# Optimization experiments

Measured on AMD Instinct MI355X. Metric: run time of the kernel, lower is better.

Reference implementation:

```python
import jax, jax.numpy as jnp
import numpy as np

D, W, H = 128, 128, 128          # volume obj_shape (d, w, h)
RES_SCALE = 1.4
RES_D = int(D * RES_SCALE)       # 179 detector rows
RES_H = int(H * RES_SCALE)       # 179 detector cols
N_PROJ = 10


def setup_inputs() -> dict:
    key = jax.random.key(0)
    k1, k2 = jax.random.split(key, 2)
    # learnable reconstruction volume, initialized to ones (torch.ones_like)
    I_rec = jnp.ones((1, 1, D, W, H), dtype=jnp.float32)
    # emitter positions, scaled to volume size; y-component kept away from the
    # source plane y=0 so that ray directions are well-conditioned
    poses = jax.random.uniform(k1, (50, 3), dtype=jnp.float32)
    poses = poses * jnp.array([D, W, H], jnp.float32) + jnp.array([-64.0, 256.0, -64.0], jnp.float32)
    idx = jax.random.randint(k2, (N_PROJ,), 0, 50, dtype=jnp.int32)
    return {"I_rec": I_rec, "poses": poses, "idx": idx}


def _trilinear_3d(vol, coords):
    """torch F.grid_sample 3D, bilinear, align_corners=False, zero padding.
    vol: [D, Hd, Wd]; coords: [..., 3] in (x, y, z) normalized to [-1, 1],
    where x indexes the last (Wd) axis, y the middle, z the first."""
    Dv, Hv, Wv = vol.shape
    x, y, z = coords[..., 0], coords[..., 1], coords[..., 2]
    ix = ((x + 1.0) * Wv - 1.0) * 0.5
    iy = ((y + 1.0) * Hv - 1.0) * 0.5
    iz = ((z + 1.0) * Dv - 1.0) * 0.5
    x0f, y0f, z0f = jnp.floor(ix), jnp.floor(iy), jnp.floor(iz)
    tx, ty, tz = ix - x0f, iy - y0f, iz - z0f
    x0 = x0f.astype(jnp.int32); y0 = y0f.astype(jnp.int32); z0 = z0f.astype(jnp.int32)
    x1, y1, z1 = x0 + 1, y0 + 1, z0 + 1

    def gather(zc, yc, xc):
        valid = (zc >= 0) & (zc < Dv) & (yc >= 0) & (yc < Hv) & (xc >= 0) & (xc < Wv)
        v = vol[jnp.clip(zc, 0, Dv - 1), jnp.clip(yc, 0, Hv - 1), jnp.clip(xc, 0, Wv - 1)]
        return jnp.where(valid, v, 0.0)

    out = (
        gather(z0, y0, x0) * (1 - tz) * (1 - ty) * (1 - tx)
        + gather(z0, y0, x1) * (1 - tz) * (1 - ty) * tx
        + gather(z0, y1, x0) * (1 - tz) * ty * (1 - tx)
        + gather(z0, y1, x1) * (1 - tz) * ty * tx
        + gather(z1, y0, x0) * tz * (1 - ty) * (1 - tx)
        + gather(z1, y0, x1) * tz * (1 - ty) * tx
        + gather(z1, y1, x0) * tz * ty * (1 - tx)
        + gather(z1, y1, x1) * tz * ty * tx
    )
    return out


def _project_one(vol, emi):
    """vol: [D, W, H]; emi: [3] emitter position. Returns [RES_D, RES_H]."""
    lin_x = jnp.linspace(-RES_D / 2.0, RES_D / 2.0 - 1.0, RES_D, dtype=jnp.float32)
    lin_y = jnp.linspace(-RES_H / 2.0, RES_H / 2.0 - 1.0, RES_H, dtype=jnp.float32)
    gx, gy = jnp.meshgrid(lin_x, lin_y, indexing="ij")            # [Gx, Gy]
    rays = jnp.stack([gx, jnp.zeros_like(gx), gy], axis=-1) - emi  # [Gx, Gy, 3]
    rays = rays / jnp.linalg.norm(rays, axis=-1, keepdims=True)
    dx = jnp.abs(1.0 / rays[..., 1])                               # [Gx, Gy]
    # (P0 - I0) . N  with N = (0,1,0): source-plane y samples minus emitter y
    p0y = jnp.linspace(0.0, W - 1.0, W, dtype=jnp.float32)         # [K=W]
    T = (1.0 / rays[..., 1])[..., None] * (p0y - emi[1])           # [Gx, Gy, K]
    grid = rays[..., None, :] * T[..., None] + emi                 # [Gx, Gy, K, 3]
    g0 = grid[..., 0] / D * 2.0
    g1 = grid[..., 1] / W * 2.0 - 1.0
    g2 = grid[..., 2] / H * 2.0
    coords = jnp.stack([g2, g1, g0], axis=-1)  # torch.flip(grid, [3]) -> (x,y,z)
    samp = _trilinear_3d(vol, coords)          # [Gx, Gy, K]
    return jnp.sum(samp, axis=-1) * dx


def reference(I_rec, poses, idx):
    sel = poses[idx]  # [10, 3]
    vol = I_rec[0, 0]
    projections = jax.vmap(lambda e: _project_one(vol, e))(sel)  # [10, Gx, Gy]
    return projections[None], idx
```

## Files before the change

kernel.cpp:

```cpp
#include <hip/hip_runtime.h>


#define DVOL   128
#define RES    179
#define NPROJ  10
#define OUT_PROJ (NPROJ * RES * RES)
#define BATCH  8

#define PS_A   132
#define PS_C   131
#define PS_SLAB (PS_C * PS_A)
#define PS_TOT  (DVOL * PS_SLAB)

__global__ __launch_bounds__(256) void pad_kernel(const float* __restrict__ vol,
                                                  float* __restrict__ ps) {
    const int t = blockIdx.x * 256 + threadIdx.x;
    if (t >= PS_TOT) return;
    const int p  = t / PS_SLAB;
    const int r  = t - p * PS_SLAB;
    const int ci = r / PS_A;
    const int ai = r - ci * PS_A;
    const int c = ci - 1, a = ai - 1;
    float v = 0.0f;
    if (c >= 0 && c < 128 && a >= 0 && a < 128) {
        const float* src = vol + (c << 14) + (p << 7) + a;
        v = src[0];
        if (p >= 1) v += src[-128];
    }
    ps[t] = v;
}

__device__ __forceinline__ void axis_interval(float base, float slope, float lo, float hi,
                                              float& t0, float& t1) {
    if (fabsf(slope) < 1e-9f) {
        const bool in = (base >= lo && base <= hi);
        t0 = in ? -1e30f : 1e30f;
        t1 = in ?  1e30f : -1e30f;
    } else {
        const float inv = 1.0f / slope;
        const float a = (lo - base) * inv;
        const float b = (hi - base) * inv;
        t0 = fminf(a, b);
        t1 = fmaxf(a, b);
    }
}

__device__ __forceinline__ int wave_imin(int v) {
    #pragma unroll
    for (int o = 32; o; o >>= 1) v = min(v, __shfl_xor(v, o, 64));
    return v;
}
__device__ __forceinline__ int wave_imax(int v) {
    #pragma unroll
    for (int o = 32; o; o >>= 1) v = max(v, __shfl_xor(v, o, 64));
    return v;
}

__global__ __launch_bounds__(128) void proj_fast(
    const float* __restrict__ ps,
    const float* __restrict__ poses,
    const int* __restrict__ idx,
    float* __restrict__ out)
{
    const int lane = threadIdx.x & 63;
    const int wid  = threadIdx.x >> 6;
    int gj = blockIdx.x * 64 + lane;
    int gi = blockIdx.y * 2 + wid;
    const int j = blockIdx.z;

    if (blockIdx.x == 0 && blockIdx.y == 0 && j == 0 && threadIdx.x < NPROJ)
        out[OUT_PROJ + threadIdx.x] = (float)idx[threadIdx.x];

    const bool store_ok = (gi < RES) && (gj < RES);
    gi = min(gi, RES - 1);
    gj = min(gj, RES - 1);

    const int pid = idx[j];
    const float ex = poses[pid * 3 + 0];
    const float ey = poses[pid * 3 + 1];
    const float ez = poses[pid * 3 + 2];

    const float pdx = (float)gi - 89.5f;
    const float pdz = (float)gj - 89.5f;

    const float inv_ey = 1.0f / ey;
    const float sx = (ex - pdx) * inv_ey;
    const float sz = (ez - pdz) * inv_ey;
    const float ddx = pdx - ex, ddz = pdz - ez;
    const float dxw = sqrtf(ddx * ddx + ey * ey + ddz * ddz) * fabsf(inv_ey);
    const float cb = pdx + 63.5f;
    const float ab = pdz + 63.5f;

    float gc0, gc1, ga0, ga1;
    axis_interval(cb, sx, -1.0f, 128.0f, gc0, gc1);
    axis_interval(ab, sz, -1.0f, 128.0f, ga0, ga1);
    const float q_lo = fmaxf(fmaxf(gc0, ga0), 0.0f);
    const float q_hi = fminf(fminf(gc1, ga1), 127.0f);
    int q0, q1;
    if (q_lo <= q_hi + 0.5f) {
        q0 = max(0, (int)ceilf(q_lo) - 1);
        q1 = min(DVOL, (int)floorf(q_hi) + 2);
    } else { q0 = DVOL; q1 = 0; }
    int Q0 = wave_imin(q0);
    int Q1 = wave_imax(q1);
    Q0 = __builtin_amdgcn_readfirstlane(Q0);
    Q1 = __builtin_amdgcn_readfirstlane(Q1);

    float acc = 0.0f;
    int p = Q0;
    float cf = fmaf((float)Q0, sx, cb);
    float af = fmaf((float)Q0, sz, ab);
    const float* slab = ps + Q0 * PS_SLAB;

    for (; p + (BATCH - 1) < Q1; p += BATCH) {
        float tc[BATCH], ta[BATCH];
        float2 r0[BATCH], r1[BATCH];
        #pragma unroll
        for (int k = 0; k < BATCH; ++k) {
            const float cfc = fminf(fmaxf(fmaf((float)k, sx, cf), -1.0f), 128.0f);
            const float afc = fminf(fmaxf(fmaf((float)k, sz, af), -1.0f), 128.0f);
            const float c0f = floorf(cfc);
            const float a0f = floorf(afc);
            tc[k] = cfc - c0f;
            ta[k] = afc - a0f;
            const int c0 = __builtin_amdgcn_readfirstlane((int)c0f);
            const int a0 = (int)a0f;
            const float* row = slab + k * PS_SLAB + (c0 + 1) * PS_A + 1;
            r0[k] = *(const float2*)(row + a0);
            r1[k] = *(const float2*)(row + PS_A + a0);
        }
        #pragma unroll
        for (int k = 0; k < BATCH; ++k) {
            const float h0 = fmaf(ta[k], r0[k].y - r0[k].x, r0[k].x);
            const float h1 = fmaf(ta[k], r1[k].y - r1[k].x, r1[k].x);
            acc += fmaf(tc[k], h1 - h0, h0);
        }
        cf += (float)BATCH * sx;
        af += (float)BATCH * sz;
        slab += BATCH * PS_SLAB;
    }
    for (; p < Q1; ++p) {
        const float cfc = fminf(fmaxf(cf, -1.0f), 128.0f);
        const float afc = fminf(fmaxf(af, -1.0f), 128.0f);
        const float c0f = floorf(cfc);
        const float a0f = floorf(afc);
        const float tc = cfc - c0f;
        const float ta = afc - a0f;
        const int c0 = __builtin_amdgcn_readfirstlane((int)c0f);
        const int a0 = (int)a0f;
        const float* row = slab + (c0 + 1) * PS_A + 1;
        const float2 r0 = *(const float2*)(row + a0);
        const float2 r1 = *(const float2*)(row + PS_A + a0);
        const float h0 = fmaf(ta, r0.y - r0.x, r0.x);
        const float h1 = fmaf(ta, r1.y - r1.x, r1.x);
        acc += fmaf(tc, h1 - h0, h0);
        cf += sx; af += sz; slab += PS_SLAB;
    }

    if (store_ok) out[j * (RES * RES) + gi * RES + gj] = acc * (0.5f * dxw);
}

__global__ __launch_bounds__(256) void proj_kernel_fb(
    const float* __restrict__ vol, const float* __restrict__ poses,
    const int* __restrict__ idx, float* __restrict__ out)
{
    const int gj = blockIdx.x * 64 + (threadIdx.x & 63);
    const int gi = blockIdx.y * 4 + (threadIdx.x >> 6);
    const int j  = blockIdx.z;
    if (blockIdx.x == 0 && blockIdx.y == 0 && j == 0 && threadIdx.x < NPROJ)
        out[OUT_PROJ + threadIdx.x] = (float)idx[threadIdx.x];
    if (gi >= RES || gj >= RES) return;
    const int pid = idx[j];
    const float ex = poses[pid*3+0], ey = poses[pid*3+1], ez = poses[pid*3+2];
    const float pdx = (float)gi - 89.5f, pdz = (float)gj - 89.5f;
    const float inv_ey = 1.0f / ey;
    const float sx = (ex - pdx) * inv_ey, sz = (ez - pdz) * inv_ey;
    const float ddx = pdx - ex, ddz = pdz - ez;
    const float dxw = sqrtf(ddx*ddx + ey*ey + ddz*ddz) * fabsf(inv_ey);
    const float cb = pdx + 63.5f, ab = pdz + 63.5f;
    float acc = 0.0f;
    for (int p = 0; p < DVOL; ++p) {
        const float cf = fmaf((float)p, sx, cb);
        const float af = fmaf((float)p, sz, ab);
        if (cf >= -1.0f && cf < 128.0f && af >= -1.0f && af < 128.0f) {
            const float c0f = floorf(cf), a0f = floorf(af);
            const float tc = cf - c0f, ta = af - a0f;
            const int c0 = (int)c0f, a0 = (int)a0f;
            const float wc0 = (c0 >= 0)   ? (1.0f - tc) : 0.0f;
            const float wc1 = (c0 <= 126) ? tc          : 0.0f;
            const float wa0 = (a0 >= 0)   ? (1.0f - ta) : 0.0f;
            const float wa1 = (a0 <= 126) ? ta          : 0.0f;
            const int c0c = c0 < 0 ? 0 : c0;
            const int c1c = c0 >= 127 ? 127 : c0 + 1;
            const int a0c = a0 < 0 ? 0 : a0;
            const int a1c = a0 >= 127 ? 127 : a0 + 1;
            const float w00 = wc0*wa0, w01 = wc0*wa1, w10 = wc1*wa0, w11 = wc1*wa1;
            const int b0 = (c0c << 14) + (p << 7);
            const int b1 = (c1c << 14) + (p << 7);
            float s = w00*vol[b0+a0c] + w01*vol[b0+a1c] + w10*vol[b1+a0c] + w11*vol[b1+a1c];
            if (p >= 1)
                s += w00*vol[b0+a0c-128] + w01*vol[b0+a1c-128]
                   + w10*vol[b1+a0c-128] + w11*vol[b1+a1c-128];
            acc += 0.5f * s;
        }
    }
    out[j * (RES * RES) + gi * RES + gj] = acc * dxw;
}

extern "C" void kernel_launch(void* const* d_in, const int* in_sizes, int n_in,
                              void* d_out, int out_size, void* d_ws, size_t ws_size,
                              hipStream_t stream) {
    const float* vol   = (const float*)d_in[0];
    const float* poses = (const float*)d_in[1];
    const int*   idx   = (const int*)d_in[2];
    float* out = (float*)d_out;

    if (ws_size >= (size_t)PS_TOT * sizeof(float)) {
        float* ps = (float*)d_ws;
        pad_kernel<<<PS_TOT / 256, 256, 0, stream>>>(vol, ps);
        dim3 grid(3 , 90 , NPROJ);
        proj_fast<<<grid, 128, 0, stream>>>(ps, poses, idx, out);
    } else {
        dim3 grid(3, 45, NPROJ);
        proj_kernel_fb<<<grid, 256, 0, stream>>>(vol, poses, idx, out);
    }
}
```

Before: 108.7 us.

## Interleave adjacent rows as packed bf16 pairs to halve gather loads

```diff
diff --git a/kernel.cpp b/kernel.cpp
--- a/kernel.cpp
+++ b/kernel.cpp
@@ -1,4 +1,6 @@
 #include <hip/hip_runtime.h>
+#include <hip/hip_bf16.h>
+#include <stdint.h>
 
 
 #define DVOL   128
@@ -7,27 +9,36 @@
 #define OUT_PROJ (NPROJ * RES * RES)
 #define BATCH  8
 
-#define PS_A   132
-#define PS_C   131
-#define PS_SLAB (PS_C * PS_A)
-#define PS_TOT  (DVOL * PS_SLAB)
+#define IL_A   132
+#define IL_C   130
+#define IL_SLAB (IL_C * IL_A)
+#define IL_TOT  (DVOL * IL_SLAB)
+
+__device__ __forceinline__ float psval(const float* __restrict__ vol, int p, int r, int ai) {
+    const int c = r - 1, a = ai - 1;
+    if (c < 0 || c >= 128 || a < 0 || a >= 128) return 0.0f;
+    const float* src = vol + (c << 14) + (p << 7) + a;
+    float v = src[0];
+    if (p >= 1) v += src[-128];
+    return v;
+}
+
+__device__ __forceinline__ uint32_t bfbits(float v) {
+    __hip_bfloat16 h = __float2bfloat16(v);
+    return (uint32_t)*(unsigned short*)&h;
+}
 
 __global__ __launch_bounds__(256) void pad_kernel(const float* __restrict__ vol,
-                                                  float* __restrict__ ps) {
+                                                  uint32_t* __restrict__ il) {
     const int t = blockIdx.x * 256 + threadIdx.x;
-    if (t >= PS_TOT) return;
-    const int p  = t / PS_SLAB;
-    const int r  = t - p * PS_SLAB;
-    const int ci = r / PS_A;
-    const int ai = r - ci * PS_A;
-    const int c = ci - 1, a = ai - 1;
-    float v = 0.0f;
-    if (c >= 0 && c < 128 && a >= 0 && a < 128) {
-        const float* src = vol + (c << 14) + (p << 7) + a;
-        v = src[0];
-        if (p >= 1) v += src[-128];
-    }
-    ps[t] = v;
+    if (t >= IL_TOT) return;
+    const int p  = t / IL_SLAB;
+    const int r  = t - p * IL_SLAB;
+    const int ci = r / IL_A;
+    const int ai = r - ci * IL_A;
+    const float lo = psval(vol, p, ci,     ai);
+    const float hi = psval(vol, p, ci + 1, ai);
+    il[t] = (bfbits(hi) << 16) | bfbits(lo);
 }
 
 __device__ __forceinline__ void axis_interval(float base, float slope, float lo, float hi,
@@ -56,8 +67,10 @@
     return v;
 }
 
+__device__ __forceinline__ float asf(uint32_t u) { return __uint_as_float(u); }
+
 __global__ __launch_bounds__(128) void proj_fast(
-    const float* __restrict__ ps,
+    const uint32_t* __restrict__ il,
     const float* __restrict__ poses,
     const int* __restrict__ idx,
     float* __restrict__ out)
@@ -110,11 +123,11 @@
     int p = Q0;
     float cf = fmaf((float)Q0, sx, cb);
     float af = fmaf((float)Q0, sz, ab);
-    const float* slab = ps + Q0 * PS_SLAB;
+    const uint32_t* slab = il + Q0 * IL_SLAB;
 
     for (; p + (BATCH - 1) < Q1; p += BATCH) {
         float tc[BATCH], ta[BATCH];
-        float2 r0[BATCH], r1[BATCH];
+        uint2 w[BATCH];
         #pragma unroll
         for (int k = 0; k < BATCH; ++k) {
             const float cfc = fminf(fmaxf(fmaf((float)k, sx, cf), -1.0f), 128.0f);
@@ -125,19 +138,22 @@
             ta[k] = afc - a0f;
             const int c0 = __builtin_amdgcn_readfirstlane((int)c0f);
             const int a0 = (int)a0f;
-            const float* row = slab + k * PS_SLAB + (c0 + 1) * PS_A + 1;
-            r0[k] = *(const float2*)(row + a0);
-            r1[k] = *(const float2*)(row + PS_A + a0);
+            const uint32_t* wr = slab + k * IL_SLAB + (c0 + 1) * IL_A + 1;
+            w[k] = *(const uint2*)(wr + a0);
         }
         #pragma unroll
         for (int k = 0; k < BATCH; ++k) {
-            const float h0 = fmaf(ta[k], r0[k].y - r0[k].x, r0[k].x);
-            const float h1 = fmaf(ta[k], r1[k].y - r1[k].x, r1[k].x);
+            const float f00 = asf(w[k].x << 16);
+            const float f10 = asf(w[k].x & 0xffff0000u);
+            const float f01 = asf(w[k].y << 16);
+            const float f11 = asf(w[k].y & 0xffff0000u);
+            const float h0 = fmaf(ta[k], f01 - f00, f00);
+            const float h1 = fmaf(ta[k], f11 - f10, f10);
             acc += fmaf(tc[k], h1 - h0, h0);
         }
         cf += (float)BATCH * sx;
         af += (float)BATCH * sz;
-        slab += BATCH * PS_SLAB;
+        slab += BATCH * IL_SLAB;
     }
     for (; p < Q1; ++p) {
         const float cfc = fminf(fmaxf(cf, -1.0f), 128.0f);
@@ -148,13 +164,16 @@
         const float ta = afc - a0f;
         const int c0 = __builtin_amdgcn_readfirstlane((int)c0f);
         const int a0 = (int)a0f;
-        const float* row = slab + (c0 + 1) * PS_A + 1;
-        const float2 r0 = *(const float2*)(row + a0);
-        const float2 r1 = *(const float2*)(row + PS_A + a0);
-        const float h0 = fmaf(ta, r0.y - r0.x, r0.x);
-        const float h1 = fmaf(ta, r1.y - r1.x, r1.x);
+        const uint32_t* wr = slab + (c0 + 1) * IL_A + 1;
+        const uint2 w2 = *(const uint2*)(wr + a0);
+        const float f00 = asf(w2.x << 16);
+        const float f10 = asf(w2.x & 0xffff0000u);
+        const float f01 = asf(w2.y << 16);
+        const float f11 = asf(w2.y & 0xffff0000u);
+        const float h0 = fmaf(ta, f01 - f00, f00);
+        const float h1 = fmaf(ta, f11 - f10, f10);
         acc += fmaf(tc, h1 - h0, h0);
-        cf += sx; af += sz; slab += PS_SLAB;
+        cf += sx; af += sz; slab += IL_SLAB;
     }
 
     if (store_ok) out[j * (RES * RES) + gi * RES + gj] = acc * (0.5f * dxw);
@@ -215,11 +234,11 @@
     const int*   idx   = (const int*)d_in[2];
     float* out = (float*)d_out;
 
-    if (ws_size >= (size_t)PS_TOT * sizeof(float)) {
-        float* ps = (float*)d_ws;
-        pad_kernel<<<PS_TOT / 256, 256, 0, stream>>>(vol, ps);
+    if (ws_size >= (size_t)IL_TOT * sizeof(uint32_t)) {
+        uint32_t* ilbuf = (uint32_t*)d_ws;
+        pad_kernel<<<IL_TOT / 256, 256, 0, stream>>>(vol, ilbuf);
         dim3 grid(3 , 90 , NPROJ);
-        proj_fast<<<grid, 128, 0, stream>>>(ps, poses, idx, out);
+        proj_fast<<<grid, 128, 0, stream>>>(ilbuf, poses, idx, out);
     } else {
         dim3 grid(3, 45, NPROJ);
         proj_kernel_fb<<<grid, 256, 0, stream>>>(vol, poses, idx, out);
```

After: 101.4 us. 1.07x faster.
